# Optimization experiments

Measured on AMD Instinct MI355X. Metric: run time of the kernel, lower is better.

Reference implementation:

```python
import jax, jax.numpy as jnp
import numpy as np

B, S, L, V = 512, 17, 81, 13030
ENC, OE, PE, H = 240, 80, 60, 200
IN = ENC + OE + PE  # 380
TEMPERATURE = 1.0


def setup_inputs() -> dict:
    key = jax.random.key(0)
    ks = jax.random.split(key, 16)
    enc = jax.random.normal(ks[0], (B, L, ENC), dtype=jnp.float32)
    in_adj_phase = jnp.zeros((B,), dtype=bool)
    loc_idxs = jax.random.randint(ks[1], (B, L), 0, S)  # which step each location decodes at
    order_masks = jax.random.bernoulli(ks[2], 0.2, (B, S, V))
    power_1h = jnp.eye(7, dtype=jnp.float32)[jax.random.randint(ks[3], (B,), 0, 7)]
    w = 0.1
    return {
        'enc': enc,
        'in_adj_phase': in_adj_phase,
        'loc_idxs': loc_idxs,
        'order_masks': order_masks,
        'power_1h': power_1h,
        'order_embedding': w * jax.random.normal(ks[4], (V, OE), dtype=jnp.float32),
        'power_W': w * jax.random.normal(ks[5], (PE, 7), dtype=jnp.float32),
        'power_b': w * jax.random.normal(ks[6], (PE,), dtype=jnp.float32),
        'W_ih': w * jax.random.normal(ks[7], (4 * H, IN), dtype=jnp.float32),
        'W_hh': w * jax.random.normal(ks[8], (4 * H, H), dtype=jnp.float32),
        'b_ih': w * jax.random.normal(ks[9], (4 * H,), dtype=jnp.float32),
        'b_hh': w * jax.random.normal(ks[10], (4 * H,), dtype=jnp.float32),
        'out_W': w * jax.random.normal(ks[11], (V, H), dtype=jnp.float32),
        'out_b': w * jax.random.normal(ks[12], (V,), dtype=jnp.float32),
        'master_alignments': jax.random.uniform(ks[13], (L, L), dtype=jnp.float32),
    }


def reference(enc, in_adj_phase, loc_idxs, order_masks, power_1h,
              order_embedding, power_W, power_b, W_ih, W_hh, b_ih, b_hh,
              out_W, out_b, master_alignments):
    # eval mode: dropout masks are not applied (self.training is False)
    power_emb = power_1h @ power_W.T + power_b  # [B, PE]
    invalid = ~jnp.any(loc_idxs != -1, axis=1)  # [B] rows with no orders to give
    keys = jax.random.split(jax.random.key(42), S)

    def step_fn(carry, xs):
        h, c, order_emb = carry
        step, mask_t, k = xs  # mask_t: [B, V]
        # alignment over locations decoded at this step
        sel = ((loc_idxs == step) | (loc_idxs == -2)).astype(enc.dtype)  # [B, L]
        align = sel @ master_alignments  # [B, L]
        denom = jnp.sum(align, axis=1, keepdims=True)
        align = jnp.where(denom != 0, align / denom, 0.0)  # NaN -> 0 as in torch
        loc_enc = jnp.einsum('bl,bld->bd', align, enc)  # [B, ENC]
        x = jnp.concatenate([loc_enc, order_emb, power_emb], axis=1)  # [B, IN]
        gates = x @ W_ih.T + b_ih + h @ W_hh.T + b_hh  # torch gate order i,f,g,o
        i, f, g, o = jnp.split(gates, 4, axis=1)
        c_new = jax.nn.sigmoid(f) * c + jax.nn.sigmoid(i) * jnp.tanh(g)
        h_new = jax.nn.sigmoid(o) * jnp.tanh(c_new)
        scores = h_new @ out_W.T + out_b  # [B, V]
        m = jnp.where(invalid[:, None], True, mask_t)
        scores = jnp.minimum(scores, m.astype(scores.dtype) * 1e9 - 1e8)
        idx = jax.random.categorical(k, scores / TEMPERATURE, axis=-1)  # [B]
        order_emb_new = order_embedding[idx]  # [B, OE]
        return (h_new, c_new, order_emb_new), (idx, scores)

    carry0 = (jnp.zeros((B, H), enc.dtype), jnp.zeros((B, H), enc.dtype),
              jnp.zeros((B, OE), enc.dtype))
    xs = (jnp.arange(S), jnp.transpose(order_masks, (1, 0, 2)), keys)
    _, (idxs, scores) = jax.lax.scan(step_fn, carry0, xs)
    return jnp.transpose(idxs, (1, 0)), jnp.transpose(scores, (1, 0, 2))
```

## Files before the change

kernel.cpp:

```cpp
#include <hip/hip_runtime.h>
#include <math.h>

#define NB 512
#define NS 17
#define NL 81
#define NV 13030
#define NENC 240
#define NOE 80
#define NPE 60
#define NH 200
#define NIN 380
#define NG 800
#define KP 224
#define KG 608
#define NVP 13056
#define NGP 832
#define NBLK 204

#define XH_ENC 224
#define XH_OE  464
#define XH_PE  544

typedef short bf8_t __attribute__((ext_vector_type(8)));
typedef float f4_t __attribute__((ext_vector_type(4)));

__device__ __forceinline__ unsigned short f2bf(float f) {
  unsigned u = __float_as_uint(f);
  unsigned r = (u + 0x7fffu + ((u >> 16) & 1u)) >> 16;
  return (unsigned short)r;
}

__device__ __host__ __forceinline__ unsigned rotl32h(unsigned x, int d) {
  return (x << d) | (x >> (32 - d));
}
__device__ __host__ __forceinline__ void threefry2x32(
    unsigned k0, unsigned k1, unsigned x0, unsigned x1,
    unsigned& y0, unsigned& y1) {
  unsigned ks2 = k0 ^ k1 ^ 0x1BD11BDAu;
  x0 += k0; x1 += k1;
#define TFR(r) { x0 += x1; x1 = rotl32h(x1, r); x1 ^= x0; }
  TFR(13) TFR(15) TFR(26) TFR(6)
  x0 += k1;  x1 += ks2 + 1u;
  TFR(17) TFR(29) TFR(16) TFR(24)
  x0 += ks2; x1 += k0 + 2u;
  TFR(13) TFR(15) TFR(26) TFR(6)
  x0 += k0;  x1 += k1 + 3u;
  TFR(17) TFR(29) TFR(16) TFR(24)
  x0 += k1;  x1 += ks2 + 4u;
  TFR(13) TFR(15) TFR(26) TFR(6)
  x0 += ks2; x1 += k0 + 5u;
#undef TFR
  y0 = x0; y1 = x1;
}

__device__ __forceinline__ float gumbel_from_bits(unsigned bits) {
  float u = __uint_as_float((bits >> 9) | 0x3f800000u) - 1.0f;
  if (u == 0.0f) u = 1.17549435e-38f;
  return -__logf(-__logf(u));
}

__global__ void __launch_bounds__(256) prep_wcat_kernel(
    const float* __restrict__ W_ih, const float* __restrict__ W_hh,
    unsigned short* __restrict__ Wcat) {
  int t = blockIdx.x * 256 + threadIdx.x;
  if (t >= NGP * KG) return;
  int n = t / KG, k = t % KG;
  float v = 0.f;
  if (n < NG) {
    if (k < NH) v = W_hh[n * NH + k];
    else if (k >= XH_ENC && k < XH_PE + NPE) v = W_ih[n * NIN + (k - XH_ENC)];
  }
  Wcat[t] = f2bf(v);
}

__global__ void __launch_bounds__(256) prep_outw_kernel(
    const float* __restrict__ out_W, unsigned short* __restrict__ outWb) {
  int t = blockIdx.x * 256 + threadIdx.x;
  if (t >= NVP * KP) return;
  int n = t / KP, k = t % KP;
  outWb[t] = f2bf((n < NV && k < NH) ? out_W[n * NH + k] : 0.f);
}

__global__ void __launch_bounds__(256) misc_kernel(
    const float* __restrict__ power_1h, const float* __restrict__ power_W,
    const float* __restrict__ power_b, const int* __restrict__ loc_idxs,
    const float* __restrict__ b_ih, const float* __restrict__ b_hh,
    unsigned short* __restrict__ xh, float* __restrict__ bcat,
    int* __restrict__ invalid) {
  int t = blockIdx.x * 256 + threadIdx.x;
  if (t < NB * NPE) {
    int b = t / NPE, p = t % NPE;
    float a = power_b[p];
#pragma unroll
    for (int k = 0; k < 7; ++k) a = fmaf(power_1h[b * 7 + k], power_W[p * 7 + k], a);
    xh[(size_t)b * KG + XH_PE + p] = f2bf(a);
  }
  if (t < NG) bcat[t] = b_ih[t] + b_hh[t];
  if (t < NB) {
    bool any = false;
    for (int l = 0; l < NL; ++l) any = any || (loc_idxs[t * NL + l] != -1);
    invalid[t] = any ? 0 : 1;
  }
}

__global__ void __launch_bounds__(256) build_x_kernel(
    const int* __restrict__ loc_idxs, const float* __restrict__ MA,
    const float* __restrict__ enc, unsigned short* __restrict__ xh, int step) {
  __shared__ float sel[NL];
  __shared__ float aln[NL];
  __shared__ float denom;
  const int b = blockIdx.x, tid = threadIdx.x;
  if (tid < NL) {
    int li = loc_idxs[b * NL + tid];
    sel[tid] = (li == step || li == -2) ? 1.0f : 0.0f;
  }
  __syncthreads();
  if (tid < NL) {
    float a = 0.f;
    for (int l = 0; l < NL; ++l) a = fmaf(sel[l], MA[l * NL + tid], a);
    aln[tid] = a;
  }
  __syncthreads();
  if (tid == 0) {
    float d = 0.f;
    for (int l = 0; l < NL; ++l) d += aln[l];
    denom = d;
  }
  __syncthreads();
  if (tid < NL) aln[tid] = (denom != 0.f) ? aln[tid] / denom : 0.0f;
  __syncthreads();
  if (tid < NENC) {
    const float* eb = enc + (size_t)b * NL * NENC + tid;
    float a = 0.f;
    for (int l = 0; l < NL; ++l) a = fmaf(aln[l], eb[(size_t)l * NENC], a);
    xh[(size_t)b * KG + XH_ENC + tid] = f2bf(a);
  }
}

__device__ __forceinline__ void mfma_nt_16x64(
    const unsigned short* __restrict__ A, const unsigned short* __restrict__ B,
    int lda, int ldb, int m0w, int n0, int nk, f4_t acc[4]) {
  const int lane = threadIdx.x & 63;
  const int tx = lane & 15, quad = lane >> 4;
  const unsigned short* ap = A + (size_t)(m0w + tx) * lda + quad * 8;
  const unsigned short* bp0 = B + (size_t)(n0 + tx) * ldb + quad * 8;
  for (int kc = 0; kc < nk; ++kc) {
    bf8_t a = *(const bf8_t*)(ap + kc * 32);
#pragma unroll
    for (int jf = 0; jf < 4; ++jf) {
      bf8_t b = *(const bf8_t*)(bp0 + (size_t)jf * 16 * ldb + kc * 32);
      acc[jf] = __builtin_amdgcn_mfma_f32_16x16x32_bf16(a, b, acc[jf], 0, 0, 0);
    }
  }
}

__global__ void __launch_bounds__(256) gates_kernel(
    const unsigned short* __restrict__ xh, const unsigned short* __restrict__ Wcat,
    const float* __restrict__ bcat, float* __restrict__ gates) {
  const int w = threadIdx.x >> 6;
  const int lane = threadIdx.x & 63;
  const int tx = lane & 15, quad = lane >> 4;
  const int m0w = blockIdx.y * 64 + w * 16;
  const int n0 = blockIdx.x * 64;
  f4_t acc[4] = {};
  mfma_nt_16x64(xh, Wcat, KG, KG, m0w, n0, KG / 32, acc);
#pragma unroll
  for (int jf = 0; jf < 4; ++jf) {
    int n = n0 + jf * 16 + tx;
    if (n >= NG) continue;
    float bias = bcat[n];
#pragma unroll
    for (int reg = 0; reg < 4; ++reg) {
      int m = m0w + quad * 4 + reg;
      gates[(size_t)m * NG + n] = acc[jf][reg] + bias;
    }
  }
}

__global__ void __launch_bounds__(256) lstm_cell_kernel(
    const float* __restrict__ gates, unsigned short* __restrict__ xh,
    float* __restrict__ c) {
  int t = blockIdx.x * 256 + threadIdx.x;
  if (t >= NB * NH) return;
  int b = t / NH, j = t % NH;
  const float* g = gates + (size_t)b * NG;
  float gi = g[j], gf = g[NH + j], gg = g[2 * NH + j], go = g[3 * NH + j];
  float si = 1.f / (1.f + expf(-gi));
  float sf = 1.f / (1.f + expf(-gf));
  float so = 1.f / (1.f + expf(-go));
  float cn = sf * c[t] + si * tanhf(gg);
  float hn = so * tanhf(cn);
  c[t] = cn;
  xh[(size_t)b * KG + j] = f2bf(hn);
}

__global__ void __launch_bounds__(256) scores_kernel(
    const unsigned short* __restrict__ xh, const unsigned short* __restrict__ outWb,
    const float* __restrict__ out_b, const int* __restrict__ order_masks,
    const int* __restrict__ invalid, float* __restrict__ out,
    float* __restrict__ pval, int* __restrict__ pidx,
    int step, unsigned k0, unsigned k1) {
  const int w = threadIdx.x >> 6;
  const int lane = threadIdx.x & 63;
  const int tx = lane & 15, quad = lane >> 4;
  const int m0w = blockIdx.y * 64 + w * 16;
  const int n0 = blockIdx.x * 64;
  f4_t acc[4] = {};
  mfma_nt_16x64(xh, outWb, KG, KP, m0w, n0, KP / 32, acc);

  float bias[4];
  int nn[4];
#pragma unroll
  for (int jf = 0; jf < 4; ++jf) {
    nn[jf] = n0 + jf * 16 + tx;
    bias[jf] = (nn[jf] < NV) ? out_b[nn[jf]] : 0.f;
  }

  float bval[4];
  int bidx[4];
#pragma unroll
  for (int reg = 0; reg < 4; ++reg) {
    const int m = m0w + quad * 4 + reg;
    const int inv = invalid[m];
    const int* mrow = order_masks + (size_t)m * NS * NV + (size_t)step * NV;
    float* orow = out + (size_t)NB * NS + ((size_t)m * NS + step) * (size_t)NV;
    float vals[4];
#pragma unroll
    for (int jf = 0; jf < 4; ++jf) {
      int n = nn[jf];
      float v = -1.0e8f;
      if (n < NV) {
        int msk = inv ? 1 : mrow[n];
        v = fminf(acc[jf][reg] + bias[jf], msk ? 9.0e8f : -1.0e8f);
        orow[n] = v;
      }
      vals[jf] = v;
    }
    unsigned base = (unsigned)m * (unsigned)NV;
    unsigned y0, y1, y2, y3;
    threefry2x32(k0, k1, base + (unsigned)nn[0], base + (unsigned)nn[1], y0, y1);
    threefry2x32(k0, k1, base + (unsigned)nn[2], base + (unsigned)nn[3], y2, y3);
    float g[4] = {gumbel_from_bits(y0), gumbel_from_bits(y1),
                  gumbel_from_bits(y2), gumbel_from_bits(y3)};
    float bv = -INFINITY; int bi = 0;
#pragma unroll
    for (int jf = 0; jf < 4; ++jf) {
      float cnd = (nn[jf] < NV) ? vals[jf] + g[jf] : -INFINITY;
      if (cnd > bv) { bv = cnd; bi = nn[jf]; }
    }
    bval[reg] = bv; bidx[reg] = bi;
  }
#pragma unroll
  for (int s = 8; s >= 1; s >>= 1) {
#pragma unroll
    for (int reg = 0; reg < 4; ++reg) {
      float ov = __shfl_xor(bval[reg], s);
      int oi = __shfl_xor(bidx[reg], s);
      if (ov > bval[reg]) { bval[reg] = ov; bidx[reg] = oi; }
    }
  }
#pragma unroll
  for (int reg = 0; reg < 4; ++reg) {
    if (tx == reg) {
      int m = m0w + quad * 4 + reg;
      pval[(size_t)m * NBLK + blockIdx.x] = bval[reg];
      pidx[(size_t)m * NBLK + blockIdx.x] = bidx[reg];
    }
  }
}

__global__ void __launch_bounds__(256) sample_kernel(
    const float* __restrict__ pval, const int* __restrict__ pidx,
    const float* __restrict__ order_embedding, unsigned short* __restrict__ xh,
    float* __restrict__ out, int step) {
  const int m = blockIdx.x, tid = threadIdx.x;
  __shared__ float sv[256];
  __shared__ int si[256];
  float v = -INFINITY; int i = 0;
  if (tid < NBLK) { v = pval[(size_t)m * NBLK + tid]; i = pidx[(size_t)m * NBLK + tid]; }
  sv[tid] = v; si[tid] = i;
  __syncthreads();
  for (int off = 128; off > 0; off >>= 1) {
    if (tid < off) {
      float v2 = sv[tid + off]; int i2 = si[tid + off];
      if (v2 > sv[tid] || (v2 == sv[tid] && i2 < si[tid])) { sv[tid] = v2; si[tid] = i2; }
    }
    __syncthreads();
  }
  if (tid == 0) out[m * NS + step] = (float)si[0];
  if (tid < NOE) {
    int idx = si[0];
    xh[(size_t)m * KG + XH_OE + tid] = f2bf(order_embedding[(size_t)idx * NOE + tid]);
  }
}

extern "C" void kernel_launch(void* const* d_in, const int* in_sizes, int n_in,
                              void* d_out, int out_size, void* d_ws, size_t ws_size,
                              hipStream_t stream) {
  const float* enc          = (const float*)d_in[0];
  const int*   loc_idxs     = (const int*)d_in[2];
  const int*   order_masks  = (const int*)d_in[3];
  const float* power_1h     = (const float*)d_in[4];
  const float* order_embedding = (const float*)d_in[5];
  const float* power_W      = (const float*)d_in[6];
  const float* power_b      = (const float*)d_in[7];
  const float* W_ih         = (const float*)d_in[8];
  const float* W_hh         = (const float*)d_in[9];
  const float* b_ih         = (const float*)d_in[10];
  const float* b_hh         = (const float*)d_in[11];
  const float* out_W        = (const float*)d_in[12];
  const float* out_b        = (const float*)d_in[13];
  const float* MA           = (const float*)d_in[14];

  float* ws      = (float*)d_ws;
  float* c       = ws;
  float* gates   = c + NB * NH;
  float* pval    = gates + NB * NG;
  float* bcat    = pval + NB * NBLK;
  int*   pidx    = (int*)(bcat + NG);
  int*   invalid = pidx + NB * NBLK;
  unsigned short* xh    = (unsigned short*)(invalid + NB);
  unsigned short* Wcat  = xh + (size_t)NB * KG;
  unsigned short* outWb = Wcat + (size_t)NGP * KG;

  float* out = (float*)d_out;

  hipMemsetAsync(xh, 0, sizeof(unsigned short) * (size_t)NB * KG, stream);
  hipMemsetAsync(c, 0, sizeof(float) * (size_t)NB * NH, stream);
  misc_kernel<<<(NB * NPE + 255) / 256, 256, 0, stream>>>(
      power_1h, power_W, power_b, loc_idxs, b_ih, b_hh, xh, bcat, invalid);
  prep_wcat_kernel<<<(NGP * KG + 255) / 256, 256, 0, stream>>>(W_ih, W_hh, Wcat);
  prep_outw_kernel<<<(NVP * KP + 255) / 256, 256, 0, stream>>>(out_W, outWb);

  unsigned key[2 * NS];
  for (unsigned i = 0; i < NS; ++i) {
    unsigned y0, y1;
    threefry2x32(0u, 42u, i, i + NS, y0, y1);
    key[2 * i] = y0;
    threefry2x32(0u, 42u, i, i + NS, y0, y1);
    key[2 * i + 1] = y1;
  }

  dim3 gGates(NGP / 64, NB / 64);
  dim3 gScores(NBLK, NB / 64);
  for (int s = 0; s < NS; ++s) {
    build_x_kernel<<<NB, 256, 0, stream>>>(loc_idxs, MA, enc, xh, s);
    gates_kernel<<<gGates, 256, 0, stream>>>(xh, Wcat, bcat, gates);
    lstm_cell_kernel<<<(NB * NH + 255) / 256, 256, 0, stream>>>(gates, xh, c);
    scores_kernel<<<gScores, 256, 0, stream>>>(
        xh, outWb, out_b, order_masks, invalid, out, pval, pidx,
        s, key[2 * s], key[2 * s + 1]);
    sample_kernel<<<NB, 256, 0, stream>>>(pval, pidx, order_embedding, xh, out, s);
  }
}
```

Baseline: 1.947 ms.

## Fuse sampling reduction, gate GEMM and LSTM cell into one per-step kernel

Merges the previous step's argmax reduction and embedding gather, the gate GEMM, and the LSTM cell update into one kernel. Each block handles 16 batch rows, and gates are kept in shared memory instead of a global buffer. This cuts two launches per step and the global round-trip for the gates. The cost is only 32 blocks for the gate GEMM, which gives low parallelism on a large GPU. The final step's sample is handled by a separate tail kernel.

New measurement: 2.236 ms. +14.9%, slower.

```diff
diff --git a/kernel.cpp b/kernel.cpp
--- a/kernel.cpp
+++ b/kernel.cpp
@@ -16,6 +16,7 @@
 #define NVP 13056
 #define NGP 832
 #define NBLK 204
+#define RPB 16
 
 #define XH_ENC 224
 #define XH_OE  464
@@ -154,44 +155,75 @@
   }
 }
 
-__global__ void __launch_bounds__(256) gates_kernel(
-    const unsigned short* __restrict__ xh, const unsigned short* __restrict__ Wcat,
-    const float* __restrict__ bcat, float* __restrict__ gates) {
-  const int w = threadIdx.x >> 6;
-  const int lane = threadIdx.x & 63;
+__global__ void __launch_bounds__(256) step_pre_kernel(
+    const float* __restrict__ pval, const int* __restrict__ pidx,
+    const float* __restrict__ order_embedding,
+    const unsigned short* __restrict__ Wcat, const float* __restrict__ bcat,
+    unsigned short* __restrict__ xh, float* __restrict__ c,
+    float* __restrict__ out, int step) {
+  const int m0 = blockIdx.x * RPB;
+  const int tid = threadIdx.x;
+  __shared__ float sG[RPB][NG + 4];
+  __shared__ int sIdx[RPB];
+
+  if (step > 0) {
+    const int r = tid >> 4, u = tid & 15;
+    const int m = m0 + r;
+    float bv = -INFINITY; int bi = 0x7fffffff;
+    for (int j = u; j < NBLK; j += 16) {
+      float v = pval[(size_t)m * NBLK + j];
+      int   i = pidx[(size_t)m * NBLK + j];
+      if (v > bv || (v == bv && i < bi)) { bv = v; bi = i; }
+    }
+#pragma unroll
+    for (int s = 8; s >= 1; s >>= 1) {
+      float ov = __shfl_xor(bv, s);
+      int   oi = __shfl_xor(bi, s);
+      if (ov > bv || (ov == bv && oi < bi)) { bv = ov; bi = oi; }
+    }
+    if (u == 0) {
+      sIdx[r] = bi;
+      out[(size_t)m * NS + (step - 1)] = (float)bi;
+    }
+    __syncthreads();
+    for (int e = tid; e < RPB * NOE; e += 256) {
+      int rr = e / NOE, k = e % NOE;
+      xh[(size_t)(m0 + rr) * KG + XH_OE + k] =
+          f2bf(order_embedding[(size_t)sIdx[rr] * NOE + k]);
+    }
+    __syncthreads();
+  }
+
+  const int w = tid >> 6, lane = tid & 63;
   const int tx = lane & 15, quad = lane >> 4;
-  const int m0w = blockIdx.y * 64 + w * 16;
-  const int n0 = blockIdx.x * 64;
-  f4_t acc[4] = {};
-  mfma_nt_16x64(xh, Wcat, KG, KG, m0w, n0, KG / 32, acc);
-#pragma unroll
-  for (int jf = 0; jf < 4; ++jf) {
-    int n = n0 + jf * 16 + tx;
-    if (n >= NG) continue;
-    float bias = bcat[n];
-#pragma unroll
-    for (int reg = 0; reg < 4; ++reg) {
-      int m = m0w + quad * 4 + reg;
-      gates[(size_t)m * NG + n] = acc[jf][reg] + bias;
-    }
-  }
-}
-
-__global__ void __launch_bounds__(256) lstm_cell_kernel(
-    const float* __restrict__ gates, unsigned short* __restrict__ xh,
-    float* __restrict__ c) {
-  int t = blockIdx.x * 256 + threadIdx.x;
-  if (t >= NB * NH) return;
-  int b = t / NH, j = t % NH;
-  const float* g = gates + (size_t)b * NG;
-  float gi = g[j], gf = g[NH + j], gg = g[2 * NH + j], go = g[3 * NH + j];
-  float si = 1.f / (1.f + expf(-gi));
-  float sf = 1.f / (1.f + expf(-gf));
-  float so = 1.f / (1.f + expf(-go));
-  float cn = sf * c[t] + si * tanhf(gg);
-  float hn = so * tanhf(cn);
-  c[t] = cn;
-  xh[(size_t)b * KG + j] = f2bf(hn);
+  for (int tile = w; tile < NGP / 64; tile += 4) {
+    f4_t acc[4] = {};
+    mfma_nt_16x64(xh, Wcat, KG, KG, m0, tile * 64, KG / 32, acc);
+#pragma unroll
+    for (int jf = 0; jf < 4; ++jf) {
+      int n = tile * 64 + jf * 16 + tx;
+      if (n >= NG) continue;
+      float bias = bcat[n];
+#pragma unroll
+      for (int reg = 0; reg < 4; ++reg)
+        sG[quad * 4 + reg][n] = acc[jf][reg] + bias;
+    }
+  }
+  __syncthreads();
+
+  for (int e = tid; e < RPB * NH; e += 256) {
+    int rr = e / NH, j = e % NH;
+    int m = m0 + rr;
+    float gi = sG[rr][j], gf = sG[rr][NH + j];
+    float gg = sG[rr][2 * NH + j], go = sG[rr][3 * NH + j];
+    float si = 1.f / (1.f + expf(-gi));
+    float sf = 1.f / (1.f + expf(-gf));
+    float so = 1.f / (1.f + expf(-go));
+    float cn = sf * c[(size_t)m * NH + j] + si * tanhf(gg);
+    float hn = so * tanhf(cn);
+    c[(size_t)m * NH + j] = cn;
+    xh[(size_t)m * KG + j] = f2bf(hn);
+  }
 }
 
 __global__ void __launch_bounds__(256) scores_kernel(
@@ -269,29 +301,26 @@
   }
 }
 
-__global__ void __launch_bounds__(256) sample_kernel(
+__global__ void __launch_bounds__(256) final_sample_kernel(
     const float* __restrict__ pval, const int* __restrict__ pidx,
-    const float* __restrict__ order_embedding, unsigned short* __restrict__ xh,
-    float* __restrict__ out, int step) {
-  const int m = blockIdx.x, tid = threadIdx.x;
-  __shared__ float sv[256];
-  __shared__ int si[256];
-  float v = -INFINITY; int i = 0;
-  if (tid < NBLK) { v = pval[(size_t)m * NBLK + tid]; i = pidx[(size_t)m * NBLK + tid]; }
-  sv[tid] = v; si[tid] = i;
-  __syncthreads();
-  for (int off = 128; off > 0; off >>= 1) {
-    if (tid < off) {
-      float v2 = sv[tid + off]; int i2 = si[tid + off];
-      if (v2 > sv[tid] || (v2 == sv[tid] && i2 < si[tid])) { sv[tid] = v2; si[tid] = i2; }
-    }
-    __syncthreads();
-  }
-  if (tid == 0) out[m * NS + step] = (float)si[0];
-  if (tid < NOE) {
-    int idx = si[0];
-    xh[(size_t)m * KG + XH_OE + tid] = f2bf(order_embedding[(size_t)idx * NOE + tid]);
-  }
+    float* __restrict__ out) {
+  const int m0 = blockIdx.x * RPB;
+  const int tid = threadIdx.x;
+  const int r = tid >> 4, u = tid & 15;
+  const int m = m0 + r;
+  float bv = -INFINITY; int bi = 0x7fffffff;
+  for (int j = u; j < NBLK; j += 16) {
+    float v = pval[(size_t)m * NBLK + j];
+    int   i = pidx[(size_t)m * NBLK + j];
+    if (v > bv || (v == bv && i < bi)) { bv = v; bi = i; }
+  }
+#pragma unroll
+  for (int s = 8; s >= 1; s >>= 1) {
+    float ov = __shfl_xor(bv, s);
+    int   oi = __shfl_xor(bi, s);
+    if (ov > bv || (ov == bv && oi < bi)) { bv = ov; bi = oi; }
+  }
+  if (u == 0) out[(size_t)m * NS + (NS - 1)] = (float)bi;
 }
 
 extern "C" void kernel_launch(void* const* d_in, const int* in_sizes, int n_in,
@@ -322,6 +351,7 @@
   unsigned short* xh    = (unsigned short*)(invalid + NB);
   unsigned short* Wcat  = xh + (size_t)NB * KG;
   unsigned short* outWb = Wcat + (size_t)NGP * KG;
+  (void)gates;
 
   float* out = (float*)d_out;
 
@@ -341,15 +371,14 @@
     key[2 * i + 1] = y1;
   }
 
-  dim3 gGates(NGP / 64, NB / 64);
   dim3 gScores(NBLK, NB / 64);
   for (int s = 0; s < NS; ++s) {
     build_x_kernel<<<NB, 256, 0, stream>>>(loc_idxs, MA, enc, xh, s);
-    gates_kernel<<<gGates, 256, 0, stream>>>(xh, Wcat, bcat, gates);
-    lstm_cell_kernel<<<(NB * NH + 255) / 256, 256, 0, stream>>>(gates, xh, c);
+    step_pre_kernel<<<NB / RPB, 256, 0, stream>>>(
+        pval, pidx, order_embedding, Wcat, bcat, xh, c, out, s);
     scores_kernel<<<gScores, 256, 0, stream>>>(
         xh, outWb, out_b, order_masks, invalid, out, pval, pidx,
         s, key[2 * s], key[2 * s + 1]);
-    sample_kernel<<<NB, 256, 0, stream>>>(pval, pidx, order_embedding, xh, out, s);
-  }
-}
+  }
+  final_sample_kernel<<<NB / RPB, 256, 0, stream>>>(pval, pidx, out);
+}
```
